# Performance work log

Measured on AMD Instinct MI355X. Metric: run time of the kernel, lower is better.

The kernel has to match this reference:

```python
import jax, jax.numpy as jnp
import numpy as np

H = 1024  # hidden size

def lstm_cell(x, h, c, Wih, Whh, b):
    # torch gate order: i, f, g, o
    g = x @ Wih.T + h @ Whh.T + b
    i, f, gg, o = jnp.split(g, 4, axis=-1)
    c = jax.nn.sigmoid(f) * c + jax.nn.sigmoid(i) * jnp.tanh(gg)
    h = jax.nn.sigmoid(o) * jnp.tanh(c)
    return h, c

def lstm_layer(x, Wih, Whh, b):
    # x: [B, S, in] -> (y [B, S, H], h_last [B, H], c_last [B, H])
    B = x.shape[0]
    h0 = jnp.zeros((B, H), x.dtype)
    def step(carry, xt):
        h, c = carry
        h, c = lstm_cell(xt, h, c, Wih, Whh, b)
        return (h, c), h
    (h, c), ys = jax.lax.scan(step, (h0, h0), jnp.swapaxes(x, 0, 1))
    return jnp.swapaxes(ys, 0, 1), h, c

def setup_inputs() -> dict:
    key = jax.random.key(0)
    ks = iter(jax.random.split(key, 24))
    V, E, B, Ss, St = 32000, 512, 32, 64, 64
    s = 0.05
    d = {
        'source': jax.random.randint(next(ks), (B, Ss), 0, V),
        'prev_outputs': jax.random.randint(next(ks), (B, St), 0, V),
        'emb': jax.random.normal(next(ks), (V, E)) * s,
        'enc_Wih0': jax.random.normal(next(ks), (4*H, E)) * s,
        'enc_Whh0': jax.random.normal(next(ks), (4*H, H)) * s,
        'enc_b0': jax.random.normal(next(ks), (4*H,)) * s,
        'enc_Wih1': jax.random.normal(next(ks), (4*H, H)) * s,
        'enc_Whh1': jax.random.normal(next(ks), (4*H, H)) * s,
        'enc_b1': jax.random.normal(next(ks), (4*H,)) * s,
        'dec_Wih0': jax.random.normal(next(ks), (4*H, E + H)) * s,
        'dec_Whh0': jax.random.normal(next(ks), (4*H, H)) * s,
        'dec_b0': jax.random.normal(next(ks), (4*H,)) * s,
        'dec_Wih1': jax.random.normal(next(ks), (4*H, H)) * s,
        'dec_Whh1': jax.random.normal(next(ks), (4*H, H)) * s,
        'dec_b1': jax.random.normal(next(ks), (4*H,)) * s,
        'Wk': jax.random.normal(next(ks), (H, H)) * s,
        'bk': jax.random.normal(next(ks), (H,)) * s,
        'Wh': jax.random.normal(next(ks), (V, H)) * s,
        'bh': jax.random.normal(next(ks), (V,)) * s,
    }
    return d

def reference(source, prev_outputs, emb, enc_Wih0, enc_Whh0, enc_b0,
              enc_Wih1, enc_Whh1, enc_b1, dec_Wih0, dec_Whh0, dec_b0,
              dec_Wih1, dec_Whh1, dec_b1, Wk, bk, Wh, bh):
    src_e = emb[source]          # [B, Ss, E]
    tgt_e = emb[prev_outputs]    # [B, St, E]
    y0, h0e, c0e = lstm_layer(src_e, enc_Wih0, enc_Whh0, enc_b0)
    enc_out, h1e, c1e = lstm_layer(y0, enc_Wih1, enc_Whh1, enc_b1)
    h = jnp.stack([h0e, h1e])    # [L, B, H]
    c = jnp.stack([c0e, c1e])
    attn_key = enc_out @ Wk.T + bk  # constant across decoder steps

    def step(carry, xt):  # xt: [B, E]
        h, c = carry
        q = h[-1]                                        # [B, H]
        scores = jnp.einsum('bh,bsh->bs', q, attn_key)   # [B, Ss]
        probs = jax.nn.softmax(scores, axis=-1)
        ctx = jnp.einsum('bs,bsh->bh', probs, enc_out)   # [B, H]
        inp = jnp.concatenate([xt, ctx], axis=-1)        # [B, E+H]
        h0n, c0n = lstm_cell(inp, h[0], c[0], dec_Wih0, dec_Whh0, dec_b0)
        h1n, c1n = lstm_cell(h0n, h[1], c[1], dec_Wih1, dec_Whh1, dec_b1)
        logits_t = h1n @ Wh.T + bh                       # [B, V]
        return (jnp.stack([h0n, h1n]), jnp.stack([c0n, c1n])), logits_t

    _, logits = jax.lax.scan(step, (h, c), jnp.swapaxes(tgt_e, 0, 1))
    return jnp.swapaxes(logits, 0, 1)  # [B, St, V]
```

## Files before the change

### kernel.cpp

```cpp
#include <hip/hip_runtime.h>
#include <cmath>

typedef short bs8 __attribute__((ext_vector_type(8)));
typedef float f32x4 __attribute__((ext_vector_type(4)));
typedef __attribute__((address_space(3))) unsigned lds_uint;
typedef __attribute__((address_space(1))) const unsigned gbl_uint;

#define NV 32000
#define SLOTH (32 * 1024)

__device__ __forceinline__ float b2f(unsigned short u) {
  union { unsigned int i; float f; } v; v.i = ((unsigned int)u) << 16; return v.f;
}
__device__ __forceinline__ unsigned short f2b(float f) {
  unsigned int u = __float_as_uint(f);
  return (unsigned short)((u + 0x7FFFu + ((u >> 16) & 1u)) >> 16);
}
__device__ __forceinline__ f32x4 mfma16(bs8 a, bs8 b, f32x4 c) {
  return __builtin_amdgcn_mfma_f32_16x16x32_bf16(a, b, c, 0, 0, 0);
}

__device__ __forceinline__ void waitN(const unsigned* slots, int n, unsigned target) {
  if (threadIdx.x < 64) {
    for (;;) {
      unsigned mn = 0xffffffffu;
      for (int i = threadIdx.x; i < n; i += 64) {
        unsigned v = __hip_atomic_load(slots + (size_t)i * 4,
                                       __ATOMIC_RELAXED, __HIP_MEMORY_SCOPE_AGENT);
        mn = mn < v ? mn : v;
      }
#pragma unroll
      for (int off = 32; off; off >>= 1) {
        unsigned o = __shfl_xor(mn, off);
        mn = mn < o ? mn : o;
      }
      if (mn >= target) break;
      __builtin_amdgcn_s_sleep(2);
    }
  }
  __syncthreads();
}
__device__ __forceinline__ void signal_slot(unsigned* slot, unsigned val) {
  __syncthreads();
  if (threadIdx.x == 0)
    __hip_atomic_store(slot, val, __ATOMIC_RELAXED, __HIP_MEMORY_SCOPE_AGENT);
}

__device__ __forceinline__ void mfma_half_lds(
    const unsigned short* __restrict__ A, const unsigned short* wl,
    f32x4& acc0, f32x4& acc1) {
  int tid = threadIdx.x;
  int w = tid >> 6, l = tid & 63;
  int col = l & 15;
  int kb = w * 256 + (l >> 4) * 8;
  const unsigned short* ap = A + (size_t)col * 1024 + kb;
  const unsigned short* wp = wl + col * 1032 + kb;
#pragma unroll
  for (int kk = 0; kk < 256; kk += 32) {
    bs8 b1 = *(const bs8*)(wp + kk);
    acc0 = mfma16(*(const bs8*)(ap + kk), b1, acc0);
    acc1 = mfma16(*(const bs8*)(ap + 16 * 1024 + kk), b1, acc1);
  }
}
__device__ __forceinline__ void red_write4(f32x4 acc0, f32x4 acc1, float (*red)[32][17]) {
  int tid = threadIdx.x;
  int w = tid >> 6, l = tid & 63, col = l & 15;
#pragma unroll
  for (int r = 0; r < 4; r++) {
    red[w][(l >> 4) * 4 + r][col] = acc0[r];
    red[w][16 + (l >> 4) * 4 + r][col] = acc1[r];
  }
  __syncthreads();
}
__device__ __forceinline__ void cell_finish4(
    int u0, float (*red)[32][17],
    const float* __restrict__ gxrow, const float* __restrict__ bias,
    const float* __restrict__ cprev,
    unsigned short* __restrict__ hout, float* __restrict__ cout) {
  int tid = threadIdx.x;
  if (tid < 128) {
    int b_ = tid >> 2, ul = tid & 3, u = u0 + ul;
    float s0 = 0.f, s1 = 0.f, s2 = 0.f, s3 = 0.f;
#pragma unroll
    for (int ww = 0; ww < 4; ww++) {
      s0 += red[ww][b_][ul];      s1 += red[ww][b_][4 + ul];
      s2 += red[ww][b_][8 + ul];  s3 += red[ww][b_][12 + ul];
    }
    if (gxrow) {
      const float* gp = gxrow + (size_t)b_ * 4096 + u;
      s0 += gp[0]; s1 += gp[1024]; s2 += gp[2048]; s3 += gp[3072];
    }
    if (bias) {
      s0 += bias[u]; s1 += bias[u + 1024]; s2 += bias[u + 2048]; s3 += bias[u + 3072];
    }
    float si = 1.f / (1.f + expf(-s0));
    float sf = 1.f / (1.f + expf(-s1));
    float tg = tanhf(s2);
    float so = 1.f / (1.f + expf(-s3));
    float cn = sf * cprev[b_ * 1024 + u] + si * tg;
    float hn = so * tanhf(cn);
    cout[b_ * 1024 + u] = cn;
    unsigned hv = (unsigned)f2b(hn);
    unsigned ho = __shfl_down(hv, 1);
    if (!(ul & 1)) {
      unsigned packed = hv | (ho << 16);
      __hip_atomic_store((unsigned*)hout + ((size_t)b_ * 512 + (u0 >> 1) + (ul >> 1)),
                         packed, __ATOMIC_RELAXED, __HIP_MEMORY_SCOPE_AGENT);
    }
  }
}

__global__ __launch_bounds__(256, 2) void enc_persist(
    const unsigned short* __restrict__ wH0, const float* __restrict__ gx0,
    unsigned short* __restrict__ y0h, float* __restrict__ c0h,
    const unsigned short* __restrict__ wE1, const unsigned short* __restrict__ wH1,
    const float* __restrict__ eb1,
    unsigned short* __restrict__ y1h, float* __restrict__ c1h,
    unsigned* __restrict__ fE, unsigned* __restrict__ fF) {
  __shared__ unsigned short wl[2][16 * 1032];
  __shared__ float red[4][32][17];
  int bid = blockIdx.x, tid = threadIdx.x;
  int lay0 = (bid < 256);
  int u0 = (bid & 255) * 4;
  {
    const unsigned short* W0 = lay0 ? wH0 : wE1;
    const unsigned short* W1 = lay0 ? wH0 : wH1;
    for (int i = tid; i < 2048; i += 256) {
      int c = i >> 7, c8 = (i & 127) * 8;
      size_t grow = (size_t)(c >> 2) * 1024 + u0 + (c & 3);
      *(bs8*)&wl[0][c * 1032 + c8] = *(const bs8*)(W0 + grow * 1024 + c8);
      *(bs8*)&wl[1][c * 1032 + c8] = *(const bs8*)(W1 + grow * 1024 + c8);
    }
    __syncthreads();
  }
  if (lay0) {
    for (int d = 0; d < 64; d++) {
      if (d > 0) waitN(fE, 256, (unsigned)d);
      f32x4 a0 = {0.f, 0.f, 0.f, 0.f}, a1 = {0.f, 0.f, 0.f, 0.f};
      mfma_half_lds(y0h + (size_t)d * SLOTH, wl[0], a0, a1);
      red_write4(a0, a1, red);
      cell_finish4(u0, red, gx0 + (size_t)d * 131072, nullptr,
                   c0h + (size_t)d * SLOTH,
                   y0h + (size_t)(d + 1) * SLOTH, c0h + (size_t)(d + 1) * SLOTH);
      signal_slot(fE + (size_t)bid * 4, (unsigned)(d + 1));
    }
  } else {
    for (int j = 0; j < 64; j++) {
      waitN(fE, 256, (unsigned)(j + 1));
      if (j > 0) waitN(fF, 256, (unsigned)j);
      f32x4 a0 = {0.f, 0.f, 0.f, 0.f}, a1 = {0.f, 0.f, 0.f, 0.f};
      mfma_half_lds(y0h + (size_t)(j + 1) * SLOTH, wl[0], a0, a1);
      mfma_half_lds(y1h + (size_t)j * SLOTH, wl[1], a0, a1);
      red_write4(a0, a1, red);
      cell_finish4(u0, red, nullptr, eb1, c1h + (size_t)j * SLOTH,
                   y1h + (size_t)(j + 1) * SLOTH, c1h + (size_t)(j + 1) * SLOTH);
      signal_slot(fF + (size_t)(bid - 256) * 4, (unsigned)(j + 1));
    }
  }
}

__global__ __launch_bounds__(256, 2) void dec_persist(
    const unsigned short* __restrict__ ak, const unsigned short* __restrict__ enc,
    const float* __restrict__ gxd,
    const unsigned short* __restrict__ wDh0, const unsigned short* __restrict__ wD0c,
    const unsigned short* __restrict__ wD1, const unsigned short* __restrict__ wDh1,
    const float* __restrict__ db1, unsigned short* __restrict__ ctxb,
    unsigned short* __restrict__ dh0, float* __restrict__ dc0,
    unsigned short* __restrict__ dh1, float* __restrict__ dc1,
    unsigned* __restrict__ flags) {
  __shared__ unsigned short wl[2][16 * 1032];
  __shared__ float red[4][32][17];
  __shared__ float qs[1024];
  __shared__ float sc[64];
  int bid = blockIdx.x, tid = threadIdx.x;
  int cell0 = (bid < 256);
  int u0 = (bid & 255) * 4;
  unsigned* fH0 = flags;
  unsigned* fH1 = flags + 1024;
  unsigned* fP  = flags + 2048;
  {
    const unsigned short* W0 = cell0 ? wDh0 : wD1;
    const unsigned short* W1 = cell0 ? wD0c : wDh1;
    for (int i = tid; i < 2048; i += 256) {
      int c = i >> 7, c8 = (i & 127) * 8;
      size_t grow = (size_t)(c >> 2) * 1024 + u0 + (c & 3);
      *(bs8*)&wl[0][c * 1032 + c8] = *(const bs8*)(W0 + grow * 1024 + c8);
      *(bs8*)&wl[1][c * 1032 + c8] = *(const bs8*)(W1 + grow * 1024 + c8);
    }
    __syncthreads();
  }
  if (cell0) {
    for (int t = 0; t < 64; t++) {
      if (t > 0) waitN(fH0, 256, (unsigned)t);
      f32x4 a0 = {0.f, 0.f, 0.f, 0.f}, a1 = {0.f, 0.f, 0.f, 0.f};
      mfma_half_lds(dh0 + (size_t)t * SLOTH, wl[0], a0, a1);
      waitN(fP, 32, (unsigned)(t + 1));
      mfma_half_lds(ctxb + (size_t)t * SLOTH, wl[1], a0, a1);
      red_write4(a0, a1, red);
      cell_finish4(u0, red, gxd + (size_t)t * 131072, nullptr,
                   dc0 + (size_t)t * SLOTH,
                   dh0 + (size_t)(t + 1) * SLOTH, dc0 + (size_t)(t + 1) * SLOTH);
      signal_slot(fH0 + (size_t)bid * 4, (unsigned)(t + 1));
    }
  } else {
    int ab = bid - 256;
    for (int t = 0; t < 64; t++) {
      if (t > 0) waitN(fH1, 256, (unsigned)t);
      if (ab < 32) {
        {
          ushort4 u4 = *(const ushort4*)(dh1 + (size_t)t * SLOTH + (size_t)ab * 1024 + tid * 4);
          qs[tid * 4 + 0] = b2f(u4.x); qs[tid * 4 + 1] = b2f(u4.y);
          qs[tid * 4 + 2] = b2f(u4.z); qs[tid * 4 + 3] = b2f(u4.w);
        }
        __syncthreads();
        int w = tid >> 6, l = tid & 63;
        for (int ss = 0; ss < 16; ss++) {
          int s = w * 16 + ss;
          const unsigned short* kr = ak + (size_t)(s * 32 + ab) * 1024;
          float p = 0.f;
#pragma unroll
          for (int i = 0; i < 4; i++) {
            int e = (l + i * 64) * 4;
            ushort4 u4 = *(const ushort4*)&kr[e];
            p += qs[e] * b2f(u4.x) + qs[e + 1] * b2f(u4.y)
               + qs[e + 2] * b2f(u4.z) + qs[e + 3] * b2f(u4.w);
          }
          for (int off = 32; off; off >>= 1) p += __shfl_down(p, off);
          if (l == 0) sc[s] = p;
        }
        __syncthreads();
        if (tid < 64) {
          float v = sc[tid], m = v;
          for (int off = 32; off; off >>= 1) m = fmaxf(m, __shfl_xor(m, off));
          float e = expf(v - m), su = e;
          for (int off = 32; off; off >>= 1) su += __shfl_xor(su, off);
          sc[tid] = e / su;
        }
        __syncthreads();
        {
          int h4 = tid * 4;
          float a0 = 0.f, a1 = 0.f, a2 = 0.f, a3 = 0.f;
#pragma unroll 8
          for (int s = 0; s < 64; s++) {
            float p = sc[s];
            ushort4 u4 = *(const ushort4*)&enc[(size_t)(s * 32 + ab) * 1024 + h4];
            a0 += p * b2f(u4.x); a1 += p * b2f(u4.y);
            a2 += p * b2f(u4.z); a3 += p * b2f(u4.w);
          }
          unsigned* cp = (unsigned*)(ctxb + (size_t)t * SLOTH) + ab * 512 + tid * 2;
          __hip_atomic_store(cp, (unsigned)f2b(a0) | ((unsigned)f2b(a1) << 16),
                             __ATOMIC_RELAXED, __HIP_MEMORY_SCOPE_AGENT);
          __hip_atomic_store(cp + 1, (unsigned)f2b(a2) | ((unsigned)f2b(a3) << 16),
                             __ATOMIC_RELAXED, __HIP_MEMORY_SCOPE_AGENT);
        }
        signal_slot(fP + (size_t)ab * 4, (unsigned)(t + 1));
      }
      f32x4 a0 = {0.f, 0.f, 0.f, 0.f}, a1 = {0.f, 0.f, 0.f, 0.f};
      mfma_half_lds(dh1 + (size_t)t * SLOTH, wl[1], a0, a1);
      waitN(fH0, 256, (unsigned)(t + 1));
      mfma_half_lds(dh0 + (size_t)(t + 1) * SLOTH, wl[0], a0, a1);
      red_write4(a0, a1, red);
      cell_finish4(u0, red, nullptr, db1, dc1 + (size_t)t * SLOTH,
                   dh1 + (size_t)(t + 1) * SLOTH, dc1 + (size_t)(t + 1) * SLOTH);
      signal_slot(fH1 + (size_t)(bid - 256) * 4, (unsigned)(t + 1));
    }
  }
}

struct CvtDesc { const float* src; unsigned short* dst; int total8, cols, ld, col0, blk0; };
struct CvtArgs { CvtDesc d[11]; };
__global__ __launch_bounds__(256) void cvt_all(CvtArgs a) {
  int blk = blockIdx.x, seg = 0;
#pragma unroll
  for (int i = 1; i < 11; i++) if (blk >= a.d[i].blk0) seg = i;
  CvtDesc d = a.d[seg];
  int idx = (blk - d.blk0) * 256 + threadIdx.x;
  if (idx >= d.total8) return;
  int cpr = d.cols >> 3;
  int r = idx / cpr, c8 = (idx - r * cpr) * 8;
  const float* s = d.src + (size_t)r * d.ld + d.col0 + c8;
  float4 x = *(const float4*)s, y = *(const float4*)(s + 4);
  unsigned short o[8] = {f2b(x.x), f2b(x.y), f2b(x.z), f2b(x.w),
                         f2b(y.x), f2b(y.y), f2b(y.z), f2b(y.w)};
  *(bs8*)(d.dst + (size_t)r * d.cols + c8) = *(bs8*)o;
}

__global__ __launch_bounds__(256) void embed_kernel(
    const int* __restrict__ src, const int* __restrict__ prev,
    const float* __restrict__ emb,
    unsigned short* __restrict__ se, unsigned short* __restrict__ te) {
  int idx = blockIdx.x * 256 + threadIdx.x;
  int half = idx >> 17;
  int r = (idx >> 6) & 2047, c8 = (idx & 63) * 8;
  int s = r >> 5, b = r & 31;
  const int* tok = half ? prev : src;
  unsigned short* dst = half ? te : se;
  int t = tok[b * 64 + s];
  const float* e = emb + (size_t)t * 512 + c8;
  float4 a = *(const float4*)e, bb = *(const float4*)(e + 4);
  unsigned short o[8] = {f2b(a.x), f2b(a.y), f2b(a.z), f2b(a.w),
                         f2b(bb.x), f2b(bb.y), f2b(bb.z), f2b(bb.w)};
  *(bs8*)(dst + (size_t)r * 512 + c8) = *(bs8*)o;
}

#define NFLAGS 6272
__global__ __launch_bounds__(256) void zero_init(
    unsigned short* y0h, unsigned short* y1h, float* c0h, float* c1h,
    unsigned* flags) {
  int i = blockIdx.x * 256 + threadIdx.x;
  y0h[i] = 0; y1h[i] = 0; c0h[i] = 0.f; c1h[i] = 0.f;
  if (i < NFLAGS) flags[i] = 0u;
}
__global__ __launch_bounds__(256) void init_dec(
    const unsigned short* __restrict__ y0f, const unsigned short* __restrict__ y1f,
    const float* __restrict__ c0f, const float* __restrict__ c1f,
    unsigned short* dh0, unsigned short* dh1, float* dc0, float* dc1) {
  int i = blockIdx.x * 256 + threadIdx.x;
  dh0[i] = y0f[i]; dh1[i] = y1f[i]; dc0[i] = c0f[i]; dc1[i] = c1f[i];
}

template <int OUTMODE>
__global__ __launch_bounds__(256) void gemm_bf16(
    const unsigned short* __restrict__ A, int lda,
    const unsigned short* __restrict__ B, int ldb,
    const float* __restrict__ bias, void* __restrict__ Cp, int ldc, int K) {
  __shared__ unsigned short As[128 * 64];
  __shared__ unsigned short Bs[128 * 64];
  int tid = threadIdx.x;
  int m0, n0;
  if (OUTMODE == 1) {
    int nwg = gridDim.x * gridDim.y;
    int orig = blockIdx.y * gridDim.x + blockIdx.x;
    int q = nwg >> 3;
    int wg = (orig & 7) * q + (orig >> 3);
    m0 = (wg % gridDim.x) * 128;
    n0 = (wg / gridDim.x) * 128;
  } else {
    m0 = blockIdx.x * 128; n0 = blockIdx.y * 128;
  }
  int w = tid >> 6, l = tid & 63;
  int wr = w >> 1, wc = w & 1;
  int swz = ((l & 7) * 8) ^ ((l >> 3) * 8);
  f32x4 acc[4][4];
#pragma unroll
  for (int i = 0; i < 4; i++)
#pragma unroll
    for (int j = 0; j < 4; j++)
#pragma unroll
      for (int r = 0; r < 4; r++) acc[i][j][r] = 0.f;

  for (int k0 = 0; k0 < K; k0 += 64) {
    __syncthreads();
#pragma unroll
    for (int i = 0; i < 4; i++) {
      int rb = w * 8 + i * 32;
      const unsigned short* ga = A + (size_t)(m0 + rb + (l >> 3)) * lda + k0 + swz;
      __builtin_amdgcn_global_load_lds((gbl_uint*)ga, (lds_uint*)&As[rb * 64], 16, 0, 0);
      const unsigned short* gb = B + (size_t)(n0 + rb + (l >> 3)) * ldb + k0 + swz;
      __builtin_amdgcn_global_load_lds((gbl_uint*)gb, (lds_uint*)&Bs[rb * 64], 16, 0, 0);
    }
    __syncthreads();
#pragma unroll
    for (int kk = 0; kk < 2; kk++) {
      bs8 af[4], bfr[4];
#pragma unroll
      for (int i = 0; i < 4; i++) {
        int R = wr * 64 + i * 16 + (l & 15);
        af[i] = *(const bs8*)&As[R * 64 + ((kk * 32 + (l >> 4) * 8) ^ ((R & 7) * 8))];
      }
#pragma unroll
      for (int j = 0; j < 4; j++) {
        int R = wc * 64 + j * 16 + (l & 15);
        bfr[j] = *(const bs8*)&Bs[R * 64 + ((kk * 32 + (l >> 4) * 8) ^ ((R & 7) * 8))];
      }
#pragma unroll
      for (int i = 0; i < 4; i++)
#pragma unroll
        for (int j = 0; j < 4; j++)
          acc[i][j] = mfma16(af[i], bfr[j], acc[i][j]);
    }
  }
#pragma unroll
  for (int i = 0; i < 4; i++) {
    int mrow = m0 + wr * 64 + i * 16 + (l >> 4) * 4;
#pragma unroll
    for (int j = 0; j < 4; j++) {
      int n = n0 + wc * 64 + j * 16 + (l & 15);
      float bb = bias ? bias[n] : 0.f;
#pragma unroll
      for (int r = 0; r < 4; r++) {
        int m = mrow + r;
        float v = acc[i][j][r] + bb;
        if (OUTMODE == 1)
          ((float*)Cp)[(size_t)(m & 31) * (64ull * NV) + (size_t)(m >> 5) * NV + n] = v;
        else if (OUTMODE == 2)
          ((unsigned short*)Cp)[(size_t)m * ldc + n] = f2b(v);
        else
          ((float*)Cp)[(size_t)m * ldc + n] = v;
      }
    }
  }
}

extern "C" void kernel_launch(void* const* d_in, const int* in_sizes, int n_in,
                              void* d_out, int out_size, void* d_ws, size_t ws_size,
                              hipStream_t stream) {
  (void)in_sizes; (void)n_in; (void)out_size; (void)ws_size;
  const int*   src   = (const int*)d_in[0];
  const int*   prev  = (const int*)d_in[1];
  const float* emb   = (const float*)d_in[2];
  const float* eWih0 = (const float*)d_in[3];
  const float* eWhh0 = (const float*)d_in[4];
  const float* eb0   = (const float*)d_in[5];
  const float* eWih1 = (const float*)d_in[6];
  const float* eWhh1 = (const float*)d_in[7];
  const float* eb1   = (const float*)d_in[8];
  const float* dWih0 = (const float*)d_in[9];
  const float* dWhh0 = (const float*)d_in[10];
  const float* db0   = (const float*)d_in[11];
  const float* dWih1 = (const float*)d_in[12];
  const float* dWhh1 = (const float*)d_in[13];
  const float* db1   = (const float*)d_in[14];
  const float* Wk    = (const float*)d_in[15];
  const float* bk    = (const float*)d_in[16];
  const float* Wh    = (const float*)d_in[17];
  const float* bh    = (const float*)d_in[18];
  float* out = (float*)d_out;

  char* p = (char*)d_ws;
  auto alloc = [&](size_t bytes) {
    char* r = p; p += (bytes + 255) & ~(size_t)255; return r;
  };
  float* gx0 = (float*)alloc(2048ull * 4096 * 4);
  float* gxd = (float*)alloc(2048ull * 4096 * 4);
  float* c0h = (float*)alloc(65ull * SLOTH * 4);
  float* c1h = (float*)alloc(65ull * SLOTH * 4);
  float* dc0 = (float*)alloc(65ull * SLOTH * 4);
  float* dc1 = (float*)alloc(65ull * SLOTH * 4);
  unsigned short* y0h  = (unsigned short*)alloc(65ull * SLOTH * 2);
  unsigned short* y1h  = (unsigned short*)alloc(65ull * SLOTH * 2);
  unsigned short* dh0  = (unsigned short*)alloc(65ull * SLOTH * 2);
  unsigned short* dh1  = (unsigned short*)alloc(65ull * SLOTH * 2);
  unsigned short* ctxb = (unsigned short*)alloc(64ull * SLOTH * 2);
  unsigned short* se   = (unsigned short*)alloc(2048ull * 512 * 2);
  unsigned short* te   = (unsigned short*)alloc(2048ull * 512 * 2);
  unsigned short* ak   = (unsigned short*)alloc(2048ull * 1024 * 2);
  unsigned short* wE0  = (unsigned short*)alloc(4096ull * 512 * 2);
  unsigned short* wH0  = (unsigned short*)alloc(4096ull * 1024 * 2);
  unsigned short* wE1  = (unsigned short*)alloc(4096ull * 1024 * 2);
  unsigned short* wH1  = (unsigned short*)alloc(4096ull * 1024 * 2);
  unsigned short* wD0x = (unsigned short*)alloc(4096ull * 512 * 2);
  unsigned short* wD0c = (unsigned short*)alloc(4096ull * 1024 * 2);
  unsigned short* wDh0 = (unsigned short*)alloc(4096ull * 1024 * 2);
  unsigned short* wD1  = (unsigned short*)alloc(4096ull * 1024 * 2);
  unsigned short* wDh1 = (unsigned short*)alloc(4096ull * 1024 * 2);
  unsigned short* wK   = (unsigned short*)alloc(1024ull * 1024 * 2);
  unsigned short* wV   = (unsigned short*)alloc((size_t)NV * 1024 * 2);
  unsigned* flags = (unsigned*)alloc((size_t)NFLAGS * 4);
  unsigned* fE = flags + 4224;
  unsigned* fF = flags + 5248;

  CvtArgs ca; int nb = 0, ci = 0;
  auto addcvt = [&](const float* s, unsigned short* d, int rows, int cols, int ld, int c0) {
    int t8 = rows * cols / 8;
    ca.d[ci++] = CvtDesc{s, d, t8, cols, ld, c0, nb};
    nb += (t8 + 255) / 256;
  };
  addcvt(eWih0, wE0, 4096, 512, 512, 0);
  addcvt(eWhh0, wH0, 4096, 1024, 1024, 0);
  addcvt(eWih1, wE1, 4096, 1024, 1024, 0);
  addcvt(eWhh1, wH1, 4096, 1024, 1024, 0);
  addcvt(dWih0, wD0x, 4096, 512, 1536, 0);
  addcvt(dWih0, wD0c, 4096, 1024, 1536, 512);
  addcvt(dWhh0, wDh0, 4096, 1024, 1024, 0);
  addcvt(dWih1, wD1, 4096, 1024, 1024, 0);
  addcvt(dWhh1, wDh1, 4096, 1024, 1024, 0);
  addcvt(Wk, wK, 1024, 1024, 1024, 0);
  addcvt(Wh, wV, NV, 1024, 1024, 0);
  cvt_all<<<nb, 256, 0, stream>>>(ca);

  zero_init<<<128, 256, 0, stream>>>(y0h, y1h, c0h, c1h, flags);
  embed_kernel<<<1024, 256, 0, stream>>>(src, prev, emb, se, te);

  gemm_bf16<0><<<dim3(16, 32), 256, 0, stream>>>(se, 512, wE0, 512, eb0, gx0, 4096, 512);
  gemm_bf16<0><<<dim3(16, 32), 256, 0, stream>>>(te, 512, wD0x, 512, db0, gxd, 4096, 512);

  enc_persist<<<512, 256, 0, stream>>>(wH0, gx0, y0h, c0h, wE1, wH1, eb1,
                                       y1h, c1h, fE, fF);

  gemm_bf16<2><<<dim3(16, 8), 256, 0, stream>>>(y1h + SLOTH, 1024, wK, 1024, bk, ak, 1024, 1024);
  init_dec<<<128, 256, 0, stream>>>(y0h + 64 * SLOTH, y1h + 64 * SLOTH,
                                    c0h + 64 * SLOTH, c1h + 64 * SLOTH,
                                    dh0, dh1, dc0, dc1);
  dec_persist<<<512, 256, 0, stream>>>(ak, y1h + SLOTH, gxd, wDh0, wD0c, wD1, wDh1,
                                       db1, ctxb, dh0, dc0, dh1, dc1, flags);
  gemm_bf16<1><<<dim3(16, 250), 256, 0, stream>>>(dh1 + SLOTH, 1024, wV, 1024, bh, out, NV, 1024);
}
```

Baseline: 2.644 ms.

## Merge decoder cell0, cell1 and attention into one 256-block persistent loop

The decoder persistent kernel drops from 512 blocks split into layer-0 and layer-1 roles to 256 blocks that each run layer 0, then layer 1, then (for 32 blocks) attention for the next step, in sequence. Only two of the four weight slices per block now stay in LDS, and the recurrent Whh weights are streamed from global memory each step. This is meant to halve block count and cut cross-role flag traffic, but it serialises the layer-1 and attention work that previously overlapped with layer 0, and it adds global weight reads inside the recurrent loop.

```diff
diff --git a/kernel.cpp b/kernel.cpp
--- a/kernel.cpp
+++ b/kernel.cpp
@@ -62,6 +62,23 @@
     acc1 = mfma16(*(const bs8*)(ap + 16 * 1024 + kk), b1, acc1);
   }
 }
+__device__ __forceinline__ void mfma_half_glb(
+    const unsigned short* __restrict__ A, const unsigned short* __restrict__ Wg,
+    int u0, f32x4& acc0, f32x4& acc1) {
+  int tid = threadIdx.x;
+  int w = tid >> 6, l = tid & 63;
+  int col = l & 15;
+  int kb = w * 256 + (l >> 4) * 8;
+  size_t wrow = (size_t)(col >> 2) * 1024 + u0 + (col & 3);
+  const unsigned short* ap = A + (size_t)col * 1024 + kb;
+  const unsigned short* wp = Wg + wrow * 1024 + kb;
+#pragma unroll
+  for (int kk = 0; kk < 256; kk += 32) {
+    bs8 b1 = *(const bs8*)(wp + kk);
+    acc0 = mfma16(*(const bs8*)(ap + kk), b1, acc0);
+    acc1 = mfma16(*(const bs8*)(ap + 16 * 1024 + kk), b1, acc1);
+  }
+}
 __device__ __forceinline__ void red_write4(f32x4 acc0, f32x4 acc1, float (*red)[32][17]) {
   int tid = threadIdx.x;
   int w = tid >> 6, l = tid & 63, col = l & 15;
@@ -72,7 +89,8 @@
   }
   __syncthreads();
 }
-__device__ __forceinline__ void cell_finish4(
+template <int NW>
+__device__ __forceinline__ void cell_finishN(
     int u0, float (*red)[32][17],
     const float* __restrict__ gxrow, const float* __restrict__ bias,
     const float* __restrict__ cprev,
@@ -82,7 +100,7 @@
     int b_ = tid >> 2, ul = tid & 3, u = u0 + ul;
     float s0 = 0.f, s1 = 0.f, s2 = 0.f, s3 = 0.f;
 #pragma unroll
-    for (int ww = 0; ww < 4; ww++) {
+    for (int ww = 0; ww < NW; ww++) {
       s0 += red[ww][b_][ul];      s1 += red[ww][b_][4 + ul];
       s2 += red[ww][b_][8 + ul];  s3 += red[ww][b_][12 + ul];
     }
@@ -139,9 +157,9 @@
       f32x4 a0 = {0.f, 0.f, 0.f, 0.f}, a1 = {0.f, 0.f, 0.f, 0.f};
       mfma_half_lds(y0h + (size_t)d * SLOTH, wl[0], a0, a1);
       red_write4(a0, a1, red);
-      cell_finish4(u0, red, gx0 + (size_t)d * 131072, nullptr,
-                   c0h + (size_t)d * SLOTH,
-                   y0h + (size_t)(d + 1) * SLOTH, c0h + (size_t)(d + 1) * SLOTH);
+      cell_finishN<4>(u0, red, gx0 + (size_t)d * 131072, nullptr,
+                      c0h + (size_t)d * SLOTH,
+                      y0h + (size_t)(d + 1) * SLOTH, c0h + (size_t)(d + 1) * SLOTH);
       signal_slot(fE + (size_t)bid * 4, (unsigned)(d + 1));
     }
   } else {
@@ -152,14 +170,69 @@
       mfma_half_lds(y0h + (size_t)(j + 1) * SLOTH, wl[0], a0, a1);
       mfma_half_lds(y1h + (size_t)j * SLOTH, wl[1], a0, a1);
       red_write4(a0, a1, red);
-      cell_finish4(u0, red, nullptr, eb1, c1h + (size_t)j * SLOTH,
-                   y1h + (size_t)(j + 1) * SLOTH, c1h + (size_t)(j + 1) * SLOTH);
+      cell_finishN<4>(u0, red, nullptr, eb1, c1h + (size_t)j * SLOTH,
+                      y1h + (size_t)(j + 1) * SLOTH, c1h + (size_t)(j + 1) * SLOTH);
       signal_slot(fF + (size_t)(bid - 256) * 4, (unsigned)(j + 1));
     }
   }
 }
 
-__global__ __launch_bounds__(256, 2) void dec_persist(
+__device__ __forceinline__ void attn_phase(
+    int ab, int tq,
+    const unsigned short* __restrict__ ak, const unsigned short* __restrict__ enc,
+    const unsigned short* __restrict__ dh1, unsigned short* __restrict__ ctxb,
+    float* qs, float* sc) {
+  int tid = threadIdx.x;
+  {
+    ushort4 u4 = *(const ushort4*)(dh1 + (size_t)tq * SLOTH + (size_t)ab * 1024 + tid * 4);
+    qs[tid * 4 + 0] = b2f(u4.x); qs[tid * 4 + 1] = b2f(u4.y);
+    qs[tid * 4 + 2] = b2f(u4.z); qs[tid * 4 + 3] = b2f(u4.w);
+  }
+  __syncthreads();
+  int w = tid >> 6, l = tid & 63;
+  for (int ss = 0; ss < 16; ss++) {
+    int s = w * 16 + ss;
+    const unsigned short* kr = ak + (size_t)(s * 32 + ab) * 1024;
+    float p = 0.f;
+#pragma unroll
+    for (int i = 0; i < 4; i++) {
+      int e = (l + i * 64) * 4;
+      ushort4 u4 = *(const ushort4*)&kr[e];
+      p += qs[e] * b2f(u4.x) + qs[e + 1] * b2f(u4.y)
+         + qs[e + 2] * b2f(u4.z) + qs[e + 3] * b2f(u4.w);
+    }
+    for (int off = 32; off; off >>= 1) p += __shfl_down(p, off);
+    if (l == 0) sc[s] = p;
+  }
+  __syncthreads();
+  if (tid < 64) {
+    float v = sc[tid], m = v;
+    for (int off = 32; off; off >>= 1) m = fmaxf(m, __shfl_xor(m, off));
+    float e = expf(v - m), su = e;
+    for (int off = 32; off; off >>= 1) su += __shfl_xor(su, off);
+    sc[tid] = e / su;
+  }
+  __syncthreads();
+  {
+    int h4 = tid * 4;
+    float a0 = 0.f, a1 = 0.f, a2 = 0.f, a3 = 0.f;
+#pragma unroll 8
+    for (int s = 0; s < 64; s++) {
+      float p = sc[s];
+      ushort4 u4 = *(const ushort4*)&enc[(size_t)(s * 32 + ab) * 1024 + h4];
+      a0 += p * b2f(u4.x); a1 += p * b2f(u4.y);
+      a2 += p * b2f(u4.z); a3 += p * b2f(u4.w);
+    }
+    unsigned* cp = (unsigned*)(ctxb + (size_t)tq * SLOTH) + ab * 512 + tid * 2;
+    __hip_atomic_store(cp, (unsigned)f2b(a0) | ((unsigned)f2b(a1) << 16),
+                       __ATOMIC_RELAXED, __HIP_MEMORY_SCOPE_AGENT);
+    __hip_atomic_store(cp + 1, (unsigned)f2b(a2) | ((unsigned)f2b(a3) << 16),
+                       __ATOMIC_RELAXED, __HIP_MEMORY_SCOPE_AGENT);
+  }
+  __syncthreads();
+}
+
+__global__ __launch_bounds__(256) void dec_persist(
     const unsigned short* __restrict__ ak, const unsigned short* __restrict__ enc,
     const float* __restrict__ gxd,
     const unsigned short* __restrict__ wDh0, const unsigned short* __restrict__ wD0c,
@@ -170,99 +243,48 @@
     unsigned* __restrict__ flags) {
   __shared__ unsigned short wl[2][16 * 1032];
   __shared__ float red[4][32][17];
-  __shared__ float qs[1024];
+  __shared__ float qs[2048];
   __shared__ float sc[64];
   int bid = blockIdx.x, tid = threadIdx.x;
-  int cell0 = (bid < 256);
-  int u0 = (bid & 255) * 4;
+  int u0 = bid * 4;
   unsigned* fH0 = flags;
   unsigned* fH1 = flags + 1024;
   unsigned* fP  = flags + 2048;
   {
-    const unsigned short* W0 = cell0 ? wDh0 : wD1;
-    const unsigned short* W1 = cell0 ? wD0c : wDh1;
     for (int i = tid; i < 2048; i += 256) {
       int c = i >> 7, c8 = (i & 127) * 8;
       size_t grow = (size_t)(c >> 2) * 1024 + u0 + (c & 3);
-      *(bs8*)&wl[0][c * 1032 + c8] = *(const bs8*)(W0 + grow * 1024 + c8);
-      *(bs8*)&wl[1][c * 1032 + c8] = *(const bs8*)(W1 + grow * 1024 + c8);
+      *(bs8*)&wl[0][c * 1032 + c8] = *(const bs8*)(wD0c + grow * 1024 + c8);
+      *(bs8*)&wl[1][c * 1032 + c8] = *(const bs8*)(wD1 + grow * 1024 + c8);
     }
     __syncthreads();
   }
-  if (cell0) {
-    for (int t = 0; t < 64; t++) {
-      if (t > 0) waitN(fH0, 256, (unsigned)t);
-      f32x4 a0 = {0.f, 0.f, 0.f, 0.f}, a1 = {0.f, 0.f, 0.f, 0.f};
-      mfma_half_lds(dh0 + (size_t)t * SLOTH, wl[0], a0, a1);
-      waitN(fP, 32, (unsigned)(t + 1));
-      mfma_half_lds(ctxb + (size_t)t * SLOTH, wl[1], a0, a1);
-      red_write4(a0, a1, red);
-      cell_finish4(u0, red, gxd + (size_t)t * 131072, nullptr,
-                   dc0 + (size_t)t * SLOTH,
-                   dh0 + (size_t)(t + 1) * SLOTH, dc0 + (size_t)(t + 1) * SLOTH);
-      signal_slot(fH0 + (size_t)bid * 4, (unsigned)(t + 1));
-    }
-  } else {
-    int ab = bid - 256;
-    for (int t = 0; t < 64; t++) {
-      if (t > 0) waitN(fH1, 256, (unsigned)t);
-      if (ab < 32) {
-        {
-          ushort4 u4 = *(const ushort4*)(dh1 + (size_t)t * SLOTH + (size_t)ab * 1024 + tid * 4);
-          qs[tid * 4 + 0] = b2f(u4.x); qs[tid * 4 + 1] = b2f(u4.y);
-          qs[tid * 4 + 2] = b2f(u4.z); qs[tid * 4 + 3] = b2f(u4.w);
-        }
-        __syncthreads();
-        int w = tid >> 6, l = tid & 63;
-        for (int ss = 0; ss < 16; ss++) {
-          int s = w * 16 + ss;
-          const unsigned short* kr = ak + (size_t)(s * 32 + ab) * 1024;
-          float p = 0.f;
-#pragma unroll
-          for (int i = 0; i < 4; i++) {
-            int e = (l + i * 64) * 4;
-            ushort4 u4 = *(const ushort4*)&kr[e];
-            p += qs[e] * b2f(u4.x) + qs[e + 1] * b2f(u4.y)
-               + qs[e + 2] * b2f(u4.z) + qs[e + 3] * b2f(u4.w);
-          }
-          for (int off = 32; off; off >>= 1) p += __shfl_down(p, off);
-          if (l == 0) sc[s] = p;
-        }
-        __syncthreads();
-        if (tid < 64) {
-          float v = sc[tid], m = v;
-          for (int off = 32; off; off >>= 1) m = fmaxf(m, __shfl_xor(m, off));
-          float e = expf(v - m), su = e;
-          for (int off = 32; off; off >>= 1) su += __shfl_xor(su, off);
-          sc[tid] = e / su;
-        }
-        __syncthreads();
-        {
-          int h4 = tid * 4;
-          float a0 = 0.f, a1 = 0.f, a2 = 0.f, a3 = 0.f;
-#pragma unroll 8
-          for (int s = 0; s < 64; s++) {
-            float p = sc[s];
-            ushort4 u4 = *(const ushort4*)&enc[(size_t)(s * 32 + ab) * 1024 + h4];
-            a0 += p * b2f(u4.x); a1 += p * b2f(u4.y);
-            a2 += p * b2f(u4.z); a3 += p * b2f(u4.w);
-          }
-          unsigned* cp = (unsigned*)(ctxb + (size_t)t * SLOTH) + ab * 512 + tid * 2;
-          __hip_atomic_store(cp, (unsigned)f2b(a0) | ((unsigned)f2b(a1) << 16),
-                             __ATOMIC_RELAXED, __HIP_MEMORY_SCOPE_AGENT);
-          __hip_atomic_store(cp + 1, (unsigned)f2b(a2) | ((unsigned)f2b(a3) << 16),
-                             __ATOMIC_RELAXED, __HIP_MEMORY_SCOPE_AGENT);
-        }
-        signal_slot(fP + (size_t)ab * 4, (unsigned)(t + 1));
-      }
-      f32x4 a0 = {0.f, 0.f, 0.f, 0.f}, a1 = {0.f, 0.f, 0.f, 0.f};
-      mfma_half_lds(dh1 + (size_t)t * SLOTH, wl[1], a0, a1);
-      waitN(fH0, 256, (unsigned)(t + 1));
-      mfma_half_lds(dh0 + (size_t)(t + 1) * SLOTH, wl[0], a0, a1);
-      red_write4(a0, a1, red);
-      cell_finish4(u0, red, nullptr, db1, dc1 + (size_t)t * SLOTH,
-                   dh1 + (size_t)(t + 1) * SLOTH, dc1 + (size_t)(t + 1) * SLOTH);
-      signal_slot(fH1 + (size_t)(bid - 256) * 4, (unsigned)(t + 1));
+  if (bid < 32) {
+    attn_phase(bid, 0, ak, enc, dh1, ctxb, qs, sc);
+    signal_slot(fP + (size_t)bid * 4, 1u);
+  }
+  for (int t = 0; t < 64; t++) {
+    waitN(fP, 32, (unsigned)(t + 1));
+    f32x4 a0 = {0.f, 0.f, 0.f, 0.f}, a1 = {0.f, 0.f, 0.f, 0.f};
+    mfma_half_glb(dh0 + (size_t)t * SLOTH, wDh0, u0, a0, a1);
+    mfma_half_lds(ctxb + (size_t)t * SLOTH, wl[0], a0, a1);
+    red_write4(a0, a1, red);
+    cell_finishN<4>(u0, red, gxd + (size_t)t * 131072, nullptr,
+                    dc0 + (size_t)t * SLOTH,
+                    dh0 + (size_t)(t + 1) * SLOTH, dc0 + (size_t)(t + 1) * SLOTH);
+    signal_slot(fH0 + (size_t)bid * 4, (unsigned)(t + 1));
+    waitN(fH0, 256, (unsigned)(t + 1));
+    f32x4 b0 = {0.f, 0.f, 0.f, 0.f}, b1 = {0.f, 0.f, 0.f, 0.f};
+    mfma_half_glb(dh1 + (size_t)t * SLOTH, wDh1, u0, b0, b1);
+    mfma_half_lds(dh0 + (size_t)(t + 1) * SLOTH, wl[1], b0, b1);
+    red_write4(b0, b1, red);
+    cell_finishN<4>(u0, red, nullptr, db1, dc1 + (size_t)t * SLOTH,
+                    dh1 + (size_t)(t + 1) * SLOTH, dc1 + (size_t)(t + 1) * SLOTH);
+    signal_slot(fH1 + (size_t)bid * 4, (unsigned)(t + 1));
+    if (bid < 32 && t < 63) {
+      waitN(fH1, 256, (unsigned)(t + 1));
+      attn_phase(bid, t + 1, ak, enc, dh1, ctxb, qs, sc);
+      signal_slot(fP + (size_t)bid * 4, (unsigned)(t + 2));
     }
   }
 }
@@ -441,7 +463,7 @@
   unsigned short* y1h  = (unsigned short*)alloc(65ull * SLOTH * 2);
   unsigned short* dh0  = (unsigned short*)alloc(65ull * SLOTH * 2);
   unsigned short* dh1  = (unsigned short*)alloc(65ull * SLOTH * 2);
-  unsigned short* ctxb = (unsigned short*)alloc(64ull * SLOTH * 2);
+  unsigned short* ctxb = (unsigned short*)alloc(65ull * SLOTH * 2);
   unsigned short* se   = (unsigned short*)alloc(2048ull * 512 * 2);
   unsigned short* te   = (unsigned short*)alloc(2048ull * 512 * 2);
   unsigned short* ak   = (unsigned short*)alloc(2048ull * 1024 * 2);
@@ -492,7 +514,7 @@
   init_dec<<<128, 256, 0, stream>>>(y0h + 64 * SLOTH, y1h + 64 * SLOTH,
                                     c0h + 64 * SLOTH, c1h + 64 * SLOTH,
                                     dh0, dh1, dc0, dc1);
-  dec_persist<<<512, 256, 0, stream>>>(ak, y1h + SLOTH, gxd, wDh0, wD0c, wD1, wDh1,
+  dec_persist<<<256, 256, 0, stream>>>(ak, y1h + SLOTH, gxd, wDh0, wD0c, wD1, wDh1,
                                        db1, ctxb, dh0, dc0, dh1, dc1, flags);
   gemm_bf16<1><<<dim3(16, 250), 256, 0, stream>>>(dh1 + SLOTH, 1024, wV, 1024, bh, out, NV, 1024);
 }
```

New measurement: 2.688 ms. About the same (+1.7%).
